# Performance work log

Hardware: AMD Instinct MI355X
Metric: run time of the kernel (lower is better)

The kernel has to match this reference:

```python
import jax, jax.numpy as jnp
import numpy as np

N = 4096
DIN = 512
H = 128    # hidden_dim per head
K = 4      # num_heads
DOUT = 16  # output classes
ALPHA = 0.2  # leaky relu negative slope


def setup_inputs() -> dict:
    key = jax.random.key(0)
    ks = jax.random.split(key, 8)
    X = jax.random.normal(ks[0], (N, DIN), jnp.float32)
    # sparse random graph (p=0.01), non-zero where edges exist
    adj = (jax.random.uniform(ks[1], (N, N)) < 0.01).astype(jnp.float32)
    W1 = jax.random.normal(ks[2], (K, DIN, H), jnp.float32) * np.float32(1.0 / np.sqrt(DIN))
    a_src1 = jax.random.normal(ks[3], (K, H), jnp.float32) * np.float32(0.1)
    a_dst1 = jax.random.normal(ks[4], (K, H), jnp.float32) * np.float32(0.1)
    W2 = jax.random.normal(ks[5], (K * H, DOUT), jnp.float32) * np.float32(1.0 / np.sqrt(K * H))
    a_src2 = jax.random.normal(ks[6], (DOUT,), jnp.float32) * np.float32(0.1)
    a_dst2 = jax.random.normal(ks[7], (DOUT,), jnp.float32) * np.float32(0.1)
    return {"X": X, "adj": adj, "W1": W1, "a_src1": a_src1, "a_dst1": a_dst1,
            "W2": W2, "a_src2": a_src2, "a_dst2": a_dst2}


def gat_multihead(h, mask, W, a_src, a_dst):
    # h: (N, Din), W: (K, Din, O), a_src/a_dst: (K, O), mask: (N, N) bool
    Wh = jnp.einsum('ni,kio->kno', h, W)                      # (K, N, O)
    src = jnp.einsum('kno,ko->kn', Wh, a_src)                 # (K, N)
    dst = jnp.einsum('kno,ko->kn', Wh, a_dst)                 # (K, N)
    e = jax.nn.leaky_relu(src[:, :, None] + dst[:, None, :], ALPHA)  # (K, N, N)
    e = jnp.where(mask[None], e, -jnp.inf)
    attn = jax.nn.softmax(e, axis=-1)                         # rows sum to 1 (self-loop guarantees >=1 edge)
    return jnp.einsum('knm,kmo->kno', attn, Wh)               # (K, N, O)


def reference(X, adj, W1, a_src1, a_dst1, W2, a_src2, a_dst2):
    # mask = (adj + I) > 0
    mask = (adj + jnp.eye(N, dtype=adj.dtype)) > 0
    # layer 1: 4 heads, concatenated, then ELU (eval mode: no dropout)
    h1 = gat_multihead(X, mask, W1, a_src1, a_dst1)           # (K, N, H)
    h1 = jnp.transpose(h1, (1, 0, 2)).reshape(N, K * H)       # concat heads -> (N, K*H)
    h1 = jax.nn.elu(h1)
    # layer 2: single head, mean over heads == the head itself
    h2 = gat_multihead(h1, mask, W2[None], a_src2[None], a_dst2[None])[0]  # (N, DOUT)
    return jax.nn.log_softmax(h2, axis=1)
```

## Files before the change

kernel.cpp:

```cpp
#include <hip/hip_runtime.h>
#include <hip/hip_bf16.h>


typedef __attribute__((ext_vector_type(4))) float floatx4;
typedef __attribute__((ext_vector_type(8))) short short8;
typedef __attribute__((ext_vector_type(4))) unsigned short ushortx4;
typedef unsigned short u16b;

#define GN 4096
#define LDP 40

__device__ __forceinline__ u16b f2bf(float f) {
  union { float f; unsigned int i; } v; v.f = f;
  unsigned int r = v.i + 0x7FFF + ((v.i >> 16) & 1);
  return (u16b)(r >> 16);
}
__device__ __forceinline__ float bflo(unsigned u) {
  union { unsigned i; float f; } v; v.i = u << 16; return v.f;
}
__device__ __forceinline__ float bfhi(unsigned u) {
  union { unsigned i; float f; } v; v.i = u & 0xffff0000u; return v.f;
}

__global__ __launch_bounds__(512) void k_fused1(const float* __restrict__ adj,
    const float* __restrict__ X, const float* __restrict__ W1,
    const float* __restrict__ as1, const float* __restrict__ ad1,
    u16b* __restrict__ csr, int* __restrict__ counts,
    u16b* __restrict__ Wh1bf, float* __restrict__ src1t, float* __restrict__ dst1t) {
  int b = blockIdx.x, t = threadIdx.x;
  int lane = t & 63, w = t >> 6;
  if (b < 512) {
    int n = b * 8 + w;
    const float* arow = adj + (size_t)n * 4096;
    u16b* row = csr + (size_t)n * 512;
    unsigned long long below = (1ull << lane) - 1ull;
    int run = 0;
#pragma unroll
    for (int ch = 0; ch < 16; ++ch) {
      int m0 = ch * 256 + lane * 4;
      floatx4 v = *(const floatx4*)(arow + m0);
      bool f0 = (v[0] != 0.f) | (m0     == n);
      bool f1 = (v[1] != 0.f) | (m0 + 1 == n);
      bool f2 = (v[2] != 0.f) | (m0 + 2 == n);
      bool f3 = (v[3] != 0.f) | (m0 + 3 == n);
      unsigned long long b0 = __ballot(f0), b1 = __ballot(f1);
      unsigned long long b2 = __ballot(f2), b3 = __ballot(f3);
      int c0 = __popcll(b0), c1 = __popcll(b1), c2 = __popcll(b2);
      if (f0) row[run +            __popcll(b0 & below)] = (u16b)m0;
      if (f1) row[run + c0 +       __popcll(b1 & below)] = (u16b)(m0 + 1);
      if (f2) row[run + c0+c1 +    __popcll(b2 & below)] = (u16b)(m0 + 2);
      if (f3) row[run + c0+c1+c2 + __popcll(b3 & below)] = (u16b)(m0 + 3);
      run += c0 + c1 + c2 + __popcll(b3);
    }
    if (lane == 0) counts[n] = run;
  } else {
    __shared__ u16b Ab[64 * LDP];
    __shared__ u16b Bb[128 * LDP];
    __shared__ float sps[4][64], sds[4][64];
    int gb = b - 512;
    int rb = (gb >> 2) * 64, hd = gb & 3;
    const float* Wk = W1 + (size_t)hd * 65536;
    int wr = w >> 2, wc = w & 3, lh = lane >> 4, lm = lane & 15;
    int ar = t >> 1, aq = t & 1;
    ar = t >> 2; aq = t & 3;
    int u = t - 256, kk0 = (u & 7) * 4, c0 = (u >> 3) * 4;
    floatx4 pa0, pa1, pb0, pb1, pb2, pb3;
    if (t < 256) {
      const float* ap = X + (size_t)(rb + ar) * 512 + aq * 8;
      pa0 = *(const floatx4*)(ap);
      pa1 = *(const floatx4*)(ap + 4);
    } else {
      const float* bp = Wk + (size_t)kk0 * 128 + c0;
      pb0 = *(const floatx4*)(bp);
      pb1 = *(const floatx4*)(bp + 128);
      pb2 = *(const floatx4*)(bp + 256);
      pb3 = *(const floatx4*)(bp + 384);
    }
    floatx4 acc[2][2] = {};
    for (int kk = 0; kk < 512; kk += 32) {
      if (t < 256) {
        short8 a;
        a[0] = (short)f2bf(pa0[0]); a[1] = (short)f2bf(pa0[1]);
        a[2] = (short)f2bf(pa0[2]); a[3] = (short)f2bf(pa0[3]);
        a[4] = (short)f2bf(pa1[0]); a[5] = (short)f2bf(pa1[1]);
        a[6] = (short)f2bf(pa1[2]); a[7] = (short)f2bf(pa1[3]);
        *(short8*)(&Ab[ar * LDP + aq * 8]) = a;
      } else {
#pragma unroll
        for (int cq = 0; cq < 4; ++cq) {
          ushortx4 v;
          v[0] = f2bf(pb0[cq]); v[1] = f2bf(pb1[cq]);
          v[2] = f2bf(pb2[cq]); v[3] = f2bf(pb3[cq]);
          *(ushortx4*)(&Bb[(c0 + cq) * LDP + kk0]) = v;
        }
      }
      __syncthreads();
      if (kk + 32 < 512) {
        if (t < 256) {
          const float* ap = X + (size_t)(rb + ar) * 512 + kk + 32 + aq * 8;
          pa0 = *(const floatx4*)(ap);
          pa1 = *(const floatx4*)(ap + 4);
        } else {
          const float* bp = Wk + (size_t)(kk + 32 + kk0) * 128 + c0;
          pb0 = *(const floatx4*)(bp);
          pb1 = *(const floatx4*)(bp + 128);
          pb2 = *(const floatx4*)(bp + 256);
          pb3 = *(const floatx4*)(bp + 384);
        }
      }
      short8 a0 = *(const short8*)(&Ab[(wr * 32      + lm) * LDP + lh * 8]);
      short8 a1 = *(const short8*)(&Ab[(wr * 32 + 16 + lm) * LDP + lh * 8]);
      short8 b0 = *(const short8*)(&Bb[(wc * 32      + lm) * LDP + lh * 8]);
      short8 b1 = *(const short8*)(&Bb[(wc * 32 + 16 + lm) * LDP + lh * 8]);
      acc[0][0] = __builtin_amdgcn_mfma_f32_16x16x32_bf16(a0, b0, acc[0][0], 0, 0, 0);
      acc[0][1] = __builtin_amdgcn_mfma_f32_16x16x32_bf16(a0, b1, acc[0][1], 0, 0, 0);
      acc[1][0] = __builtin_amdgcn_mfma_f32_16x16x32_bf16(a1, b0, acc[1][0], 0, 0, 0);
      acc[1][1] = __builtin_amdgcn_mfma_f32_16x16x32_bf16(a1, b1, acc[1][1], 0, 0, 0);
      __syncthreads();
    }
#pragma unroll
    for (int m = 0; m < 2; ++m)
#pragma unroll
      for (int n2 = 0; n2 < 2; ++n2)
#pragma unroll
        for (int j = 0; j < 4; ++j)
          Wh1bf[(size_t)(rb + wr * 32 + m * 16 + lh * 4 + j) * 512
                + hd * 128 + wc * 32 + n2 * 16 + lm] = f2bf(acc[m][n2][j]);
    float asv[2], adv[2];
#pragma unroll
    for (int n2 = 0; n2 < 2; ++n2) {
      asv[n2] = as1[hd * 128 + wc * 32 + n2 * 16 + lm];
      adv[n2] = ad1[hd * 128 + wc * 32 + n2 * 16 + lm];
    }
#pragma unroll
    for (int m = 0; m < 2; ++m)
#pragma unroll
      for (int j = 0; j < 4; ++j) {
        float ps = acc[m][0][j] * asv[0] + acc[m][1][j] * asv[1];
        float pd = acc[m][0][j] * adv[0] + acc[m][1][j] * adv[1];
#pragma unroll
        for (int off = 8; off >= 1; off >>= 1) {
          ps += __shfl_xor(ps, off, 16);
          pd += __shfl_xor(pd, off, 16);
        }
        if (lm == 0) {
          sps[wc][wr * 32 + m * 16 + lh * 4 + j] = ps;
          sds[wc][wr * 32 + m * 16 + lh * 4 + j] = pd;
        }
      }
    __syncthreads();
    if (t < 64) {
      src1t[(size_t)(rb + t) * 4 + hd] = sps[0][t] + sps[1][t] + sps[2][t] + sps[3][t];
      dst1t[(size_t)(rb + t) * 4 + hd] = sds[0][t] + sds[1][t] + sds[2][t] + sds[3][t];
    }
  }
}

__global__ __launch_bounds__(256) void k_attn1(const u16b* __restrict__ csr,
    const int* __restrict__ counts, const u16b* __restrict__ Wh1bf,
    const float* __restrict__ src1t, const float* __restrict__ dst1t,
    const float* __restrict__ W2, const float* __restrict__ as2,
    const float* __restrict__ ad2, float* __restrict__ Wh2,
    float* __restrict__ src2, float* __restrict__ dst2) {
  int n = blockIdx.x, t = threadIdx.x, lane = t & 63, w = t >> 6;
  __shared__ u16b lst[512];
  __shared__ float ew[4][516];
  __shared__ float h1row[512];
  __shared__ float redw[4][16];
  int cnt = counts[n];
  const u16b* row = csr + (size_t)n * 512;
  for (int i = t; i < cnt; i += 256) lst[i] = row[i];
  float sn[4];
#pragma unroll
  for (int k = 0; k < 4; ++k) sn[k] = src1t[n * 4 + k];
  __syncthreads();
  for (int j = t; j < cnt * 4; j += 256) {
    int li = j >> 2, k = j & 3;
    int m = lst[li];
    float e = sn[k] + dst1t[m * 4 + k];
    ew[k][li] = e > 0.f ? e : 0.2f * e;
  }
  __syncthreads();
  {
    float mx = -1e30f, sm = 0.f;
    for (int li = lane; li < cnt; li += 64) {
      float e = ew[w][li];
      if (e > mx) { sm = sm * __expf(mx - e) + 1.f; mx = e; }
      else sm += __expf(e - mx);
    }
#pragma unroll
    for (int off = 32; off >= 1; off >>= 1) {
      float mo = __shfl_xor(mx, off);
      float so = __shfl_xor(sm, off);
      float M = fmaxf(mx, mo);
      sm = sm * __expf(mx - M) + so * __expf(mo - M);
      mx = M;
    }
    float R = 1.f / sm;
    for (int li = lane; li < cnt; li += 64)
      ew[w][li] = __expf(ew[w][li] - mx) * R;
  }
  __syncthreads();
  float a0 = 0.f, a1 = 0.f;
  const float* ewk = ew[w];
#pragma unroll 4
  for (int li = 0; li < cnt; ++li) {
    int m = lst[li];
    float wv = ewk[li];
    unsigned uu = *(const unsigned*)(Wh1bf + (size_t)m * 512 + 2 * t);
    a0 = fmaf(wv, bflo(uu), a0);
    a1 = fmaf(wv, bfhi(uu), a1);
  }
  a0 = a0 > 0.f ? a0 : __expf(a0) - 1.f;
  a1 = a1 > 0.f ? a1 : __expf(a1) - 1.f;
  h1row[2 * t] = a0;
  h1row[2 * t + 1] = a1;
  __syncthreads();
  {
    int o = lane & 15, ig = lane >> 4;
    float accw = 0.f;
    for (int i = w * 128 + ig; i < (w + 1) * 128; i += 4)
      accw = fmaf(h1row[i], W2[i * 16 + o], accw);
    accw += __shfl_xor(accw, 16);
    accw += __shfl_xor(accw, 32);
    if (lane < 16) redw[w][o] = accw;
  }
  __syncthreads();
  if (t < 16) {
    float v = redw[0][t] + redw[1][t] + redw[2][t] + redw[3][t];
    Wh2[n * 16 + t] = v;
    float ps = v * as2[t];
    float pd = v * ad2[t];
#pragma unroll
    for (int off = 8; off >= 1; off >>= 1) {
      ps += __shfl_xor(ps, off, 16);
      pd += __shfl_xor(pd, off, 16);
    }
    if (t == 0) { src2[n] = ps; dst2[n] = pd; }
  }
}

__global__ __launch_bounds__(256) void k_attn2(const u16b* __restrict__ csr,
    const int* __restrict__ counts, const float* __restrict__ Wh2,
    const float* __restrict__ src2, const float* __restrict__ dst2,
    float* __restrict__ out) {
  int w = threadIdx.x >> 6, lane = threadIdx.x & 63;
  int n = blockIdx.x * 4 + w;
  int cnt = counts[n];
  const u16b* row = csr + (size_t)n * 512;
  float snv = src2[n];
  float mx = -1e30f, sm = 0.f;
  for (int li = lane; li < cnt; li += 64) {
    int m = row[li];
    float e = snv + dst2[m]; e = e > 0.f ? e : 0.2f * e;
    if (e > mx) { sm = sm * __expf(mx - e) + 1.f; mx = e; }
    else sm += __expf(e - mx);
  }
#pragma unroll
  for (int off = 32; off >= 1; off >>= 1) {
    float mo = __shfl_xor(mx, off);
    float so = __shfl_xor(sm, off);
    float M = fmaxf(mx, mo);
    sm = sm * __expf(mx - M) + so * __expf(mo - M);
    mx = M;
  }
  float R = 1.f / sm;
  int o = lane & 15, g = lane >> 4;
  float acc = 0.f;
  for (int li = g; li < cnt; li += 4) {
    int m = row[li];
    float e = snv + dst2[m]; e = e > 0.f ? e : 0.2f * e;
    float wgt = __expf(e - mx) * R;
    acc = fmaf(wgt, Wh2[m * 16 + o], acc);
  }
  acc += __shfl_xor(acc, 16);
  acc += __shfl_xor(acc, 32);
  float vm = acc;
#pragma unroll
  for (int off = 8; off >= 1; off >>= 1) vm = fmaxf(vm, __shfl_xor(vm, off, 16));
  float ex = __expf(acc - vm);
#pragma unroll
  for (int off = 8; off >= 1; off >>= 1) ex += __shfl_xor(ex, off, 16);
  if (lane < 16) out[(size_t)n * 16 + lane] = acc - vm - __logf(ex);
}

extern "C" void kernel_launch(void* const* d_in, const int* in_sizes, int n_in,
                              void* d_out, int out_size, void* d_ws, size_t ws_size,
                              hipStream_t stream) {
  const float* X   = (const float*)d_in[0];
  const float* adj = (const float*)d_in[1];
  const float* W1  = (const float*)d_in[2];
  const float* as1 = (const float*)d_in[3];
  const float* ad1 = (const float*)d_in[4];
  const float* W2  = (const float*)d_in[5];
  const float* as2 = (const float*)d_in[6];
  const float* ad2 = (const float*)d_in[7];
  float* out = (float*)d_out;

  char* ws = (char*)d_ws;
  int*   counts= (int*)ws;
  float* src1t = (float*)(ws + (16 << 10));
  float* dst1t = (float*)(ws + (80 << 10));
  float* src2  = (float*)(ws + (144 << 10));
  float* dst2  = (float*)(ws + (160 << 10));
  float* Wh2   = (float*)(ws + (176 << 10));
  u16b*  Wh1bf = (u16b*)(ws + (1ull << 20));
  u16b*  csr   = (u16b*)(ws + (5ull << 20));

  k_fused1<<<dim3(768), dim3(512), 0, stream>>>(adj, X, W1, as1, ad1,
                                                csr, counts, Wh1bf, src1t, dst1t);
  k_attn1<<<dim3(GN), dim3(256), 0, stream>>>(csr, counts, Wh1bf, src1t, dst1t,
                                              W2, as2, ad2, Wh2, src2, dst2);
  k_attn2<<<dim3(1024), dim3(256), 0, stream>>>(csr, counts, Wh2, src2, dst2, out);
}
```

Before: 68.43 us.

## Replace per-row CSR build with bitmask adjacency and in-kernel list decoding

The first kernel now packs the adjacency matrix into a bitmask of 16 bits per thread, with the self-loop bit set, instead of building a compacted CSR list with ballots and scattered stores. Both attention kernels rebuild each row's neighbor list in shared memory from the bitmask using popcount and a prefix scan. The launch grid is also reshaped (2304 blocks, with the GEMM blocks first and a remapped block-to-tile order). This removes the serialized ballot and scatter pass and shrinks the intermediate buffer, at the cost of extra decode work repeated in both attention kernels.

```diff
diff --git a/kernel.cpp b/kernel.cpp
--- a/kernel.cpp
+++ b/kernel.cpp
@@ -25,44 +25,38 @@
 __global__ __launch_bounds__(512) void k_fused1(const float* __restrict__ adj,
     const float* __restrict__ X, const float* __restrict__ W1,
     const float* __restrict__ as1, const float* __restrict__ ad1,
-    u16b* __restrict__ csr, int* __restrict__ counts,
-    u16b* __restrict__ Wh1bf, float* __restrict__ src1t, float* __restrict__ dst1t) {
+    u16b* __restrict__ mask, u16b* __restrict__ Wh1bf,
+    float* __restrict__ src1t, float* __restrict__ dst1t) {
   int b = blockIdx.x, t = threadIdx.x;
   int lane = t & 63, w = t >> 6;
-  if (b < 512) {
-    int n = b * 8 + w;
-    const float* arow = adj + (size_t)n * 4096;
-    u16b* row = csr + (size_t)n * 512;
-    unsigned long long below = (1ull << lane) - 1ull;
-    int run = 0;
-#pragma unroll
-    for (int ch = 0; ch < 16; ++ch) {
-      int m0 = ch * 256 + lane * 4;
-      floatx4 v = *(const floatx4*)(arow + m0);
-      bool f0 = (v[0] != 0.f) | (m0     == n);
-      bool f1 = (v[1] != 0.f) | (m0 + 1 == n);
-      bool f2 = (v[2] != 0.f) | (m0 + 2 == n);
-      bool f3 = (v[3] != 0.f) | (m0 + 3 == n);
-      unsigned long long b0 = __ballot(f0), b1 = __ballot(f1);
-      unsigned long long b2 = __ballot(f2), b3 = __ballot(f3);
-      int c0 = __popcll(b0), c1 = __popcll(b1), c2 = __popcll(b2);
-      if (f0) row[run +            __popcll(b0 & below)] = (u16b)m0;
-      if (f1) row[run + c0 +       __popcll(b1 & below)] = (u16b)(m0 + 1);
-      if (f2) row[run + c0+c1 +    __popcll(b2 & below)] = (u16b)(m0 + 2);
-      if (f3) row[run + c0+c1+c2 + __popcll(b3 & below)] = (u16b)(m0 + 3);
-      run += c0 + c1 + c2 + __popcll(b3);
-    }
-    if (lane == 0) counts[n] = run;
+  if (b >= 256) {
+    int n = (b - 256) * 2 + (t >> 8);
+    int cg = t & 255;
+    const float* ap = adj + (size_t)n * 4096 + cg * 16;
+    floatx4 v0 = *(const floatx4*)(ap);
+    floatx4 v1 = *(const floatx4*)(ap + 4);
+    floatx4 v2 = *(const floatx4*)(ap + 8);
+    floatx4 v3 = *(const floatx4*)(ap + 12);
+    unsigned bits = 0;
+#pragma unroll
+    for (int i = 0; i < 4; ++i) {
+      bits |= (unsigned)(v0[i] != 0.f) << i;
+      bits |= (unsigned)(v1[i] != 0.f) << (4 + i);
+      bits |= (unsigned)(v2[i] != 0.f) << (8 + i);
+      bits |= (unsigned)(v3[i] != 0.f) << (12 + i);
+    }
+    if ((n >> 4) == cg) bits |= 1u << (n & 15);
+    mask[(size_t)n * 256 + cg] = (u16b)bits;
   } else {
     __shared__ u16b Ab[64 * LDP];
     __shared__ u16b Bb[128 * LDP];
     __shared__ float sps[4][64], sds[4][64];
-    int gb = b - 512;
-    int rb = (gb >> 2) * 64, hd = gb & 3;
+    int p = ((b >> 5) << 3) | (b & 7);
+    int hd = (b >> 3) & 3;
+    int rb = p * 64;
     const float* Wk = W1 + (size_t)hd * 65536;
     int wr = w >> 2, wc = w & 3, lh = lane >> 4, lm = lane & 15;
-    int ar = t >> 1, aq = t & 1;
-    ar = t >> 2; aq = t & 3;
+    int ar = t >> 2, aq = t & 3;
     int u = t - 256, kk0 = (u & 7) * 4, c0 = (u >> 3) * 4;
     floatx4 pa0, pa1, pb0, pb1, pb2, pb3;
     if (t < 256) {
@@ -156,8 +150,8 @@
   }
 }
 
-__global__ __launch_bounds__(256) void k_attn1(const u16b* __restrict__ csr,
-    const int* __restrict__ counts, const u16b* __restrict__ Wh1bf,
+__global__ __launch_bounds__(256) void k_attn1(const u16b* __restrict__ mask,
+    const u16b* __restrict__ Wh1bf,
     const float* __restrict__ src1t, const float* __restrict__ dst1t,
     const float* __restrict__ W2, const float* __restrict__ as2,
     const float* __restrict__ ad2, float* __restrict__ Wh2,
@@ -167,12 +161,29 @@
   __shared__ float ew[4][516];
   __shared__ float h1row[512];
   __shared__ float redw[4][16];
-  int cnt = counts[n];
-  const u16b* row = csr + (size_t)n * 512;
-  for (int i = t; i < cnt; i += 256) lst[i] = row[i];
+  __shared__ int wtot[4];
+  unsigned M = mask[(size_t)n * 256 + t];
+  int pc = __popc(M);
+  int incl = pc;
+#pragma unroll
+  for (int off = 1; off <= 32; off <<= 1) {
+    int v = __shfl_up(incl, off);
+    if (lane >= off) incl += v;
+  }
+  if (lane == 63) wtot[w] = incl;
   float sn[4];
 #pragma unroll
   for (int k = 0; k < 4; ++k) sn[k] = src1t[n * 4 + k];
+  __syncthreads();
+  int base = 0;
+  for (int w2 = 0; w2 < w; ++w2) base += wtot[w2];
+  int cnt = wtot[0] + wtot[1] + wtot[2] + wtot[3];
+  int pos = base + incl - pc;
+  while (M) {
+    int c = __builtin_ctz(M);
+    lst[pos++] = (u16b)(t * 16 + c);
+    M &= M - 1;
+  }
   __syncthreads();
   for (int j = t; j < cnt * 4; j += 256) {
     int li = j >> 2, k = j & 3;
@@ -192,9 +203,9 @@
     for (int off = 32; off >= 1; off >>= 1) {
       float mo = __shfl_xor(mx, off);
       float so = __shfl_xor(sm, off);
-      float M = fmaxf(mx, mo);
-      sm = sm * __expf(mx - M) + so * __expf(mo - M);
-      mx = M;
+      float Mx = fmaxf(mx, mo);
+      sm = sm * __expf(mx - Mx) + so * __expf(mo - Mx);
+      mx = Mx;
     }
     float R = 1.f / sm;
     for (int li = lane; li < cnt; li += 64)
@@ -240,18 +251,32 @@
   }
 }
 
-__global__ __launch_bounds__(256) void k_attn2(const u16b* __restrict__ csr,
-    const int* __restrict__ counts, const float* __restrict__ Wh2,
-    const float* __restrict__ src2, const float* __restrict__ dst2,
-    float* __restrict__ out) {
+__global__ __launch_bounds__(256) void k_attn2(const u16b* __restrict__ mask,
+    const float* __restrict__ Wh2, const float* __restrict__ src2,
+    const float* __restrict__ dst2, float* __restrict__ out) {
   int w = threadIdx.x >> 6, lane = threadIdx.x & 63;
   int n = blockIdx.x * 4 + w;
-  int cnt = counts[n];
-  const u16b* row = csr + (size_t)n * 512;
+  __shared__ u16b lst4[4][512];
+  u16b* lst = lst4[w];
+  unsigned long long B = *(const unsigned long long*)((const char*)mask + (size_t)n * 512 + lane * 8);
+  int pc = __popcll(B);
+  int incl = pc;
+#pragma unroll
+  for (int off = 1; off <= 32; off <<= 1) {
+    int v = __shfl_up(incl, off);
+    if (lane >= off) incl += v;
+  }
+  int cnt = __shfl(incl, 63);
+  int pos = incl - pc;
+  while (B) {
+    int c = __builtin_ctzll(B);
+    lst[pos++] = (u16b)(lane * 64 + c);
+    B &= B - 1;
+  }
   float snv = src2[n];
   float mx = -1e30f, sm = 0.f;
   for (int li = lane; li < cnt; li += 64) {
-    int m = row[li];
+    int m = lst[li];
     float e = snv + dst2[m]; e = e > 0.f ? e : 0.2f * e;
     if (e > mx) { sm = sm * __expf(mx - e) + 1.f; mx = e; }
     else sm += __expf(e - mx);
@@ -268,7 +293,7 @@
   int o = lane & 15, g = lane >> 4;
   float acc = 0.f;
   for (int li = g; li < cnt; li += 4) {
-    int m = row[li];
+    int m = lst[li];
     float e = snv + dst2[m]; e = e > 0.f ? e : 0.2f * e;
     float wgt = __expf(e - mx) * R;
     acc = fmaf(wgt, Wh2[m * 16 + o], acc);
@@ -298,18 +323,17 @@
   float* out = (float*)d_out;
 
   char* ws = (char*)d_ws;
-  int*   counts= (int*)ws;
-  float* src1t = (float*)(ws + (16 << 10));
-  float* dst1t = (float*)(ws + (80 << 10));
-  float* src2  = (float*)(ws + (144 << 10));
-  float* dst2  = (float*)(ws + (160 << 10));
-  float* Wh2   = (float*)(ws + (176 << 10));
-  u16b*  Wh1bf = (u16b*)(ws + (1ull << 20));
-  u16b*  csr   = (u16b*)(ws + (5ull << 20));
-
-  k_fused1<<<dim3(768), dim3(512), 0, stream>>>(adj, X, W1, as1, ad1,
-                                                csr, counts, Wh1bf, src1t, dst1t);
-  k_attn1<<<dim3(GN), dim3(256), 0, stream>>>(csr, counts, Wh1bf, src1t, dst1t,
+  float* src1t = (float*)ws;
+  float* dst1t = (float*)(ws + (64 << 10));
+  float* src2  = (float*)(ws + (128 << 10));
+  float* dst2  = (float*)(ws + (144 << 10));
+  float* Wh2   = (float*)(ws + (160 << 10));
+  u16b*  mask  = (u16b*)(ws + (512 << 10));
+  u16b*  Wh1bf = (u16b*)(ws + (4ull << 20));
+
+  k_fused1<<<dim3(2304), dim3(512), 0, stream>>>(adj, X, W1, as1, ad1,
+                                                 mask, Wh1bf, src1t, dst1t);
+  k_attn1<<<dim3(GN), dim3(256), 0, stream>>>(mask, Wh1bf, src1t, dst1t,
                                               W2, as2, ad2, Wh2, src2, dst2);
-  k_attn2<<<dim3(1024), dim3(256), 0, stream>>>(csr, counts, Wh2, src2, dst2, out);
-}
+  k_attn2<<<dim3(1024), dim3(256), 0, stream>>>(mask, Wh2, src2, dst2, out);
+}
```

New measurement: 67.00 us. 2.1% less time.
